# Optimization experiments

Hardware: AMD Instinct MI355X
Metric: run time of the kernel (lower is better)

The kernel has to match this reference:

```python
import jax, jax.numpy as jnp
import numpy as np

DIM = 256
QK_DIM = 256
NUM_HEADS = 8
N_WIN = 7
TOPK = 4
SCALE = QK_DIM ** (-0.5)


def setup_inputs() -> dict:
    key = jax.random.key(0)
    k1, k2, k3 = jax.random.split(key, 3)
    N, D, H, W, C = 2, 8, 56, 56, DIM
    x = jax.random.normal(k1, (N, D, H, W, C), dtype=jnp.float32)
    # QKVLinear: Linear(dim, qk_dim + qk_dim + dim)
    Wqkv = jax.random.normal(k2, (C, 2 * QK_DIM + DIM), dtype=jnp.float32) * 0.02
    bqkv = jnp.zeros((2 * QK_DIM + DIM,), dtype=jnp.float32)
    Wo = jax.random.normal(k3, (DIM, DIM), dtype=jnp.float32) * 0.02
    bo = jnp.zeros((DIM,), dtype=jnp.float32)
    return {"x": x, "Wqkv": Wqkv, "bqkv": bqkv, "Wo": Wo, "bo": bo}


def reference(x, Wqkv, bqkv, Wo, bo):
    N, D, H, W, C = x.shape
    j = i = N_WIN
    h, w = H // j, W // i
    p2, w2 = j * i, h * w
    n = N * D
    m = NUM_HEADS
    ch = QK_DIM // m   # qk head dim
    cv = DIM // m      # v head dim

    # n t (j h) (i w) c -> n t (j i) h w c
    xw = x.reshape(N, D, j, h, i, w, C).transpose(0, 1, 2, 4, 3, 5, 6)
    xw = xw.reshape(N, D, p2, h, w, C)

    # QKVLinear then split into q / kv
    qkv = xw @ Wqkv + bqkv                       # (N,D,p2,h,w,2qk+dim)
    q = qkv[..., :QK_DIM]                        # (N,D,p2,h,w,qk)
    kv = qkv[..., QK_DIM:]                       # (N,D,p2,h,w,qk+dim)

    # inter-frame shift: frame t uses kv of frame t+1; last frame keeps its own
    kv = jnp.concatenate([kv[:, 1:], kv[:, -1:]], axis=1)

    q = q.reshape(n, p2, h, w, QK_DIM)
    kv = kv.reshape(n, p2, h, w, QK_DIM + DIM)
    q_pix = q.reshape(n, p2, w2, QK_DIM)
    kv_pix = kv.reshape(n, p2, w2, QK_DIM + DIM)  # identity kv_down

    # window-level routing (diff_routing=False -> detached)
    q_win = jax.lax.stop_gradient(q.mean(axis=(2, 3)))                  # (n,p2,qk)
    k_win = jax.lax.stop_gradient(kv[..., :QK_DIM].mean(axis=(2, 3)))   # (n,p2,qk)
    attn_logit = jnp.einsum('npc,nqc->npq', q_win * SCALE, k_win)       # (n,p2,p2)
    topk_logit, r_idx = jax.lax.top_k(attn_logit, TOPK)                 # (n,p2,topk)
    r_weight = jax.nn.softmax(topk_logit, axis=-1)  # computed, unused (mul_weight='none')

    # gather kv of routed windows: (n,p2,topk,w2,qk+dim)
    kv_sel = jax.vmap(lambda kvp, idx: kvp[idx])(kv_pix, r_idx)

    k_sel = kv_sel[..., :QK_DIM].reshape(n, p2, TOPK * w2, m, ch)
    v_sel = kv_sel[..., QK_DIM:].reshape(n, p2, TOPK * w2, m, cv)
    qh = q_pix.reshape(n, p2, w2, m, ch)

    attn = jnp.einsum('npqmc,npkmc->npmqk', qh * SCALE, k_sel)  # (n,p2,m,w2,topk*w2)
    attn = jax.nn.softmax(attn, axis=-1)
    out = jnp.einsum('npmqk,npkmc->npqmc', attn, v_sel).reshape(n, p2, w2, C)

    # (n j i) (h w) c -> N D (j h) (i w) c
    out = out.reshape(N, D, j, i, h, w, C).transpose(0, 1, 2, 4, 3, 5, 6)
    out = out.reshape(N, D, H, W, C)
    out = out @ Wo + bo
    return out
```

## Files before the change

### kernel.cpp

```cpp
#include <hip/hip_runtime.h>
#include <math.h>

#define SCALE 0.0625f

typedef __attribute__((ext_vector_type(8))) short bf16x8;
typedef __attribute__((ext_vector_type(4))) float f32x4;

__device__ __forceinline__ ushort f2bf(float f) {
    unsigned u = __float_as_uint(f);
    return (ushort)((u + 0x7FFFu + ((u >> 16) & 1u)) >> 16);
}

__device__ __forceinline__ int token_to_xrow(int t) {
    int nd  = t / 3136;
    int r   = t % 3136;
    int p   = r >> 6;
    int pix = r & 63;
    int j = p / 7, i = p % 7;
    int hh = pix >> 3, ww = pix & 7;
    return nd * 3136 + (j * 8 + hh) * 56 + (i * 8 + ww);
}

__global__ __launch_bounds__(256) void k_cast_x(const float* __restrict__ x,
                                                ushort* __restrict__ xg) {
    int gid = blockIdx.x * 256 + threadIdx.x;
    int t = gid >> 6, c = (gid & 63) * 4;
    float4 v = *(const float4*)&x[(size_t)token_to_xrow(t) * 256 + c];
    ushort4 o;
    o.x = f2bf(v.x); o.y = f2bf(v.y); o.z = f2bf(v.z); o.w = f2bf(v.w);
    *(ushort4*)&xg[(size_t)t * 256 + c] = o;
}

__global__ __launch_bounds__(256) void k_cast_w(const float* __restrict__ Wqkv,
                                                const float* __restrict__ Wo,
                                                ushort* __restrict__ Wqkvt,
                                                ushort* __restrict__ Wot) {
    int b = blockIdx.x, tid = threadIdx.x;
    if (b < 768) Wqkvt[b * 256 + tid] = f2bf(Wqkv[(size_t)tid * 768 + b]);
    else { int n = b - 768; Wot[n * 256 + tid] = f2bf(Wo[(size_t)tid * 256 + n]); }
}

__global__ __launch_bounds__(256) void k_xmean(const float* __restrict__ x,
                                               float* __restrict__ xmean) {
    int b = blockIdx.x;
    int nd = b / 49, p = b % 49;
    int j = p / 7, i = p % 7;
    const float* xb = x + ((size_t)nd * 3136 + (j * 8) * 56 + i * 8) * 256 + threadIdx.x;
    float s = 0.f;
#pragma unroll
    for (int hh = 0; hh < 8; ++hh)
#pragma unroll
        for (int ww = 0; ww < 8; ++ww) s += xb[(size_t)(hh * 56 + ww) * 256];
    xmean[(size_t)b * 256 + threadIdx.x] = s * (1.f / 64.f);
}

__global__ __launch_bounds__(256) void k_winproj(const float* __restrict__ xmean,
                                                 const float* __restrict__ Wqkv,
                                                 const float* __restrict__ bqkv,
                                                 float* __restrict__ qwin,
                                                 float* __restrict__ kwin) {
    __shared__ float As[16 * 68];
    __shared__ float Bs[16 * 64];
    const int tid = threadIdx.x;
    const int m0 = blockIdx.y * 64;
    const int n0 = blockIdx.x * 64;

    const int ar = tid >> 2;
    const int ak = (tid & 3) * 4;
    const int arow = (m0 + ar < 784) ? (m0 + ar) : 783;
    const float* aptr = xmean + (size_t)arow * 256 + ak;

    const int bk = tid >> 4;
    const int bn = (tid & 15) * 4;
    const float* bptr = Wqkv + (size_t)bk * 768 + n0 + bn;

    const int ty = tid >> 4, tx = tid & 15;
    float acc[4][4] = {};

    for (int kt = 0; kt < 256; kt += 16) {
        float4 av = *(const float4*)(aptr + kt);
        float4 bv = *(const float4*)(bptr + (size_t)kt * 768);
        __syncthreads();
        As[(ak + 0) * 68 + ar] = av.x;
        As[(ak + 1) * 68 + ar] = av.y;
        As[(ak + 2) * 68 + ar] = av.z;
        As[(ak + 3) * 68 + ar] = av.w;
        *(float4*)&Bs[bk * 64 + bn] = bv;
        __syncthreads();
#pragma unroll
        for (int kk = 0; kk < 16; ++kk) {
            float4 a4 = *(const float4*)&As[kk * 68 + ty * 4];
            float4 b4 = *(const float4*)&Bs[kk * 64 + tx * 4];
            float a[4] = {a4.x, a4.y, a4.z, a4.w};
            float b[4] = {b4.x, b4.y, b4.z, b4.w};
#pragma unroll
            for (int ii = 0; ii < 4; ++ii)
#pragma unroll
                for (int jj = 0; jj < 4; ++jj) acc[ii][jj] += a[ii] * b[jj];
        }
    }
#pragma unroll
    for (int ii = 0; ii < 4; ++ii) {
        int t = m0 + ty * 4 + ii;
        if (t >= 784) continue;
#pragma unroll
        for (int jj = 0; jj < 4; ++jj) {
            int col = n0 + tx * 4 + jj;
            float v = acc[ii][jj] + bqkv[col];
            if (col < 256) qwin[(size_t)t * 256 + col] = v;
            else           kwin[(size_t)t * 256 + (col - 256)] = v;
        }
    }
}

__global__ __launch_bounds__(64) void k_route(const float* __restrict__ qwin,
                                              const float* __restrict__ kwin,
                                              int* __restrict__ ridx) {
    const int b = blockIdx.x;
    const int nd = b / 49;
    const int ndkv = ((nd & 7) == 7) ? nd : nd + 1;
    const int t = threadIdx.x;
    __shared__ float qs[256];
    for (int i = t; i < 256; i += 64) qs[i] = qwin[b * 256 + i];
    __syncthreads();
    float logit = -INFINITY;
    if (t < 49) {
        const float* kr = kwin + ((size_t)ndkv * 49 + t) * 256;
        float s = 0.f;
        for (int c = 0; c < 256; ++c) s += qs[c] * kr[c];
        logit = s;
    }
    for (int sel = 0; sel < 4; ++sel) {
        float v = logit;
        int ix = t;
        for (int off = 32; off > 0; off >>= 1) {
            float ov = __shfl_xor(v, off);
            int   oi = __shfl_xor(ix, off);
            if (ov > v || (ov == v && oi < ix)) { v = ov; ix = oi; }
        }
        if (t == 0) ridx[b * 4 + sel] = ix;
        if (t == ix) logit = -INFINITY;
    }
}

__global__ __launch_bounds__(256) void k_gemm_qkv(const ushort* __restrict__ A,
                                                  const ushort* __restrict__ Bt,
                                                  const float* __restrict__ bqkv,
                                                  ushort* __restrict__ q,
                                                  ushort* __restrict__ kv) {
    __shared__ ushort As[128 * 32];
    __shared__ ushort Bs[128 * 32];
    const int tid = threadIdx.x;
    const int wv = tid >> 6, ln = tid & 63;
    const int lane15 = ln & 15, quad = ln >> 4;
    const int m0 = blockIdx.y * 128, n0 = blockIdx.x * 128;

    const int row0 = tid >> 2, ck = tid & 3;

    f32x4 acc[4][4];
#pragma unroll
    for (int i = 0; i < 4; ++i)
#pragma unroll
        for (int j = 0; j < 4; ++j) acc[i][j] = (f32x4){0.f, 0.f, 0.f, 0.f};

    bf16x8 avA[2], avB[2];
#pragma unroll
    for (int p = 0; p < 2; ++p) {
        avA[p] = *(const bf16x8*)(A  + (size_t)(m0 + p * 64 + row0) * 256 + ck * 8);
        avB[p] = *(const bf16x8*)(Bt + (size_t)(n0 + p * 64 + row0) * 256 + ck * 8);
    }

    const int mb = (wv >> 1) * 64, nb = (wv & 1) * 64;

    for (int kt = 0; kt < 8; ++kt) {
        __syncthreads();
#pragma unroll
        for (int p = 0; p < 2; ++p) {
            *(bf16x8*)&As[(p * 256 + tid) * 8] = avA[p];
            *(bf16x8*)&Bs[(p * 256 + tid) * 8] = avB[p];
        }
        if (kt < 7) {
#pragma unroll
            for (int p = 0; p < 2; ++p) {
                avA[p] = *(const bf16x8*)(A  + (size_t)(m0 + p * 64 + row0) * 256 + (kt + 1) * 32 + ck * 8);
                avB[p] = *(const bf16x8*)(Bt + (size_t)(n0 + p * 64 + row0) * 256 + (kt + 1) * 32 + ck * 8);
            }
        }
        __syncthreads();
        bf16x8 aF[4], bF[4];
#pragma unroll
        for (int mt = 0; mt < 4; ++mt)
            aF[mt] = *(const bf16x8*)&As[(mb + mt * 16 + lane15) * 32 + quad * 8];
#pragma unroll
        for (int nt = 0; nt < 4; ++nt)
            bF[nt] = *(const bf16x8*)&Bs[(nb + nt * 16 + lane15) * 32 + quad * 8];
#pragma unroll
        for (int mt = 0; mt < 4; ++mt)
#pragma unroll
            for (int nt = 0; nt < 4; ++nt)
                acc[mt][nt] = __builtin_amdgcn_mfma_f32_16x16x32_bf16(aF[mt], bF[nt], acc[mt][nt], 0, 0, 0);
    }

#pragma unroll
    for (int mt = 0; mt < 4; ++mt) {
#pragma unroll
        for (int nt = 0; nt < 4; ++nt) {
            int col = n0 + nb + nt * 16 + lane15;
            float bias = bqkv[col];
#pragma unroll
            for (int r = 0; r < 4; ++r) {
                int t = m0 + mb + mt * 16 + quad * 4 + r;
                ushort b = f2bf(acc[mt][nt][r] + bias);
                if (col < 256) q[(size_t)t * 256 + col] = b;
                else           kv[(size_t)t * 512 + (col - 256)] = b;
            }
        }
    }
}

__global__ __launch_bounds__(256) void k_gemm_o(const ushort* __restrict__ A,
                                                const ushort* __restrict__ Bt,
                                                const float* __restrict__ bo,
                                                float* __restrict__ out) {
    __shared__ ushort As[128 * 32];
    __shared__ ushort Bs[128 * 32];
    const int tid = threadIdx.x;
    const int wv = tid >> 6, ln = tid & 63;
    const int lane15 = ln & 15, quad = ln >> 4;
    const int m0 = blockIdx.y * 128, n0 = blockIdx.x * 128;
    const int row0 = tid >> 2, ck = tid & 3;

    f32x4 acc[4][4];
#pragma unroll
    for (int i = 0; i < 4; ++i)
#pragma unroll
        for (int j = 0; j < 4; ++j) acc[i][j] = (f32x4){0.f, 0.f, 0.f, 0.f};

    bf16x8 avA[2], avB[2];
#pragma unroll
    for (int p = 0; p < 2; ++p) {
        avA[p] = *(const bf16x8*)(A  + (size_t)(m0 + p * 64 + row0) * 256 + ck * 8);
        avB[p] = *(const bf16x8*)(Bt + (size_t)(n0 + p * 64 + row0) * 256 + ck * 8);
    }
    const int mb = (wv >> 1) * 64, nb = (wv & 1) * 64;

    for (int kt = 0; kt < 8; ++kt) {
        __syncthreads();
#pragma unroll
        for (int p = 0; p < 2; ++p) {
            *(bf16x8*)&As[(p * 256 + tid) * 8] = avA[p];
            *(bf16x8*)&Bs[(p * 256 + tid) * 8] = avB[p];
        }
        if (kt < 7) {
#pragma unroll
            for (int p = 0; p < 2; ++p) {
                avA[p] = *(const bf16x8*)(A  + (size_t)(m0 + p * 64 + row0) * 256 + (kt + 1) * 32 + ck * 8);
                avB[p] = *(const bf16x8*)(Bt + (size_t)(n0 + p * 64 + row0) * 256 + (kt + 1) * 32 + ck * 8);
            }
        }
        __syncthreads();
        bf16x8 aF[4], bF[4];
#pragma unroll
        for (int mt = 0; mt < 4; ++mt)
            aF[mt] = *(const bf16x8*)&As[(mb + mt * 16 + lane15) * 32 + quad * 8];
#pragma unroll
        for (int nt = 0; nt < 4; ++nt)
            bF[nt] = *(const bf16x8*)&Bs[(nb + nt * 16 + lane15) * 32 + quad * 8];
#pragma unroll
        for (int mt = 0; mt < 4; ++mt)
#pragma unroll
            for (int nt = 0; nt < 4; ++nt)
                acc[mt][nt] = __builtin_amdgcn_mfma_f32_16x16x32_bf16(aF[mt], bF[nt], acc[mt][nt], 0, 0, 0);
    }

#pragma unroll
    for (int mt = 0; mt < 4; ++mt) {
#pragma unroll
        for (int nt = 0; nt < 4; ++nt) {
            int col = n0 + nb + nt * 16 + lane15;
            float bias = bo[col];
#pragma unroll
            for (int r = 0; r < 4; ++r) {
                int t = m0 + mb + mt * 16 + quad * 4 + r;
                int xr = token_to_xrow(t);
                out[(size_t)xr * 256 + col] = acc[mt][nt][r] + bias;
            }
        }
    }
}

__global__ __launch_bounds__(256, 3) void k_attn(ushort* qbuf,
                                                 const ushort* __restrict__ kvbuf,
                                                 const int* __restrict__ ridx) {
    const int h = blockIdx.x, p = blockIdx.y, nd = blockIdx.z;
    const int ndkv = ((nd & 7) == 7) ? nd : nd + 1;
    const int tid = threadIdx.x;
    const int wv = tid >> 6, ln = tid & 63;
    const int lane15 = ln & 15, quad = ln >> 4;

    __shared__ ushort Ks[256 * 32];
    __shared__ ushort Vt[32 * 272];
    __shared__ ushort Ps[64 * 72];

    const int rb = (nd * 49 + p) * 4;
    int wid[4];
#pragma unroll
    for (int i = 0; i < 4; ++i) wid[i] = ridx[rb + i];

    const size_t kvband = (size_t)ndkv * 49;

    {
        int pix = tid >> 2, ck = tid & 3;
#pragma unroll
        for (int i = 0; i < 4; ++i) {
            size_t trow = (kvband + wid[i]) * 64 + pix;
            bf16x8 v = *(const bf16x8*)(kvbuf + trow * 512 + h * 32 + ck * 8);
            *(bf16x8*)&Ks[(i * 64 + pix) * 32 + ck * 8] = v;
        }
    }
    {
        int key_l = (tid & 31) * 2;
        int ch0 = (tid >> 5) * 4;
#pragma unroll
        for (int i = 0; i < 4; ++i) {
            size_t trow = (kvband + wid[i]) * 64;
            const ushort* g0 = kvbuf + (trow + key_l) * 512 + 256 + h * 32 + ch0;
            const ushort* g1 = g0 + 512;
            ushort4 a = *(const ushort4*)g0;
            ushort4 b = *(const ushort4*)g1;
            int kg = i * 64 + key_l;
            *(unsigned*)&Vt[(ch0 + 0) * 272 + kg] = (unsigned)a.x | ((unsigned)b.x << 16);
            *(unsigned*)&Vt[(ch0 + 1) * 272 + kg] = (unsigned)a.y | ((unsigned)b.y << 16);
            *(unsigned*)&Vt[(ch0 + 2) * 272 + kg] = (unsigned)a.z | ((unsigned)b.z << 16);
            *(unsigned*)&Vt[(ch0 + 3) * 272 + kg] = (unsigned)a.w | ((unsigned)b.w << 16);
        }
    }

    const size_t qrow0 = (size_t)(nd * 49 + p) * 64;
    bf16x8 bQ = *(const bf16x8*)(qbuf + (qrow0 + wv * 16 + lane15) * 256 + h * 32 + quad * 8);

    __syncthreads();

    f32x4 st[16];
#pragma unroll
    for (int t = 0; t < 16; ++t) {
        bf16x8 aK = *(const bf16x8*)&Ks[(t * 16 + lane15) * 32 + quad * 8];
        st[t] = __builtin_amdgcn_mfma_f32_16x16x32_bf16(aK, bQ, (f32x4){0.f, 0.f, 0.f, 0.f}, 0, 0, 0);
    }

    float mx = -1e30f;
#pragma unroll
    for (int t = 0; t < 16; ++t)
#pragma unroll
        for (int r = 0; r < 4; ++r) mx = fmaxf(mx, st[t][r]);
    mx = fmaxf(mx, __shfl_xor(mx, 16));
    mx = fmaxf(mx, __shfl_xor(mx, 32));
    float sum = 0.f;
#pragma unroll
    for (int t = 0; t < 16; ++t)
#pragma unroll
        for (int r = 0; r < 4; ++r) {
            float e = __expf((st[t][r] - mx) * SCALE);
            st[t][r] = e;
            sum += e;
        }
    sum += __shfl_xor(sum, 16);
    sum += __shfl_xor(sum, 32);
    const float inv = 1.f / sum;

    f32x4 oacc[2] = {{0.f, 0.f, 0.f, 0.f}, {0.f, 0.f, 0.f, 0.f}};
    const int prow = (wv * 16 + lane15) * 72;
#pragma unroll
    for (int cc = 0; cc < 4; ++cc) {
#pragma unroll
        for (int tt = 0; tt < 4; ++tt) {
            int t = cc * 4 + tt;
            unsigned lo = (unsigned)f2bf(st[t][0] * inv) | ((unsigned)f2bf(st[t][1] * inv) << 16);
            unsigned hi = (unsigned)f2bf(st[t][2] * inv) | ((unsigned)f2bf(st[t][3] * inv) << 16);
            uint2 pk; pk.x = lo; pk.y = hi;
            *(uint2*)&Ps[prow + tt * 16 + quad * 4] = pk;
        }
#pragma unroll
        for (int kt = 0; kt < 2; ++kt) {
            bf16x8 aP = *(const bf16x8*)&Ps[prow + kt * 32 + quad * 8];
#pragma unroll
            for (int nt = 0; nt < 2; ++nt) {
                bf16x8 bV = *(const bf16x8*)&Vt[(nt * 16 + lane15) * 272 + cc * 64 + kt * 32 + quad * 8];
                oacc[nt] = __builtin_amdgcn_mfma_f32_16x16x32_bf16(aP, bV, oacc[nt], 0, 0, 0);
            }
        }
    }

#pragma unroll
    for (int nt = 0; nt < 2; ++nt)
#pragma unroll
        for (int r = 0; r < 4; ++r) {
            int row = wv * 16 + quad * 4 + r;
            qbuf[(qrow0 + row) * 256 + h * 32 + nt * 16 + lane15] = f2bf(oacc[nt][r]);
        }
}

extern "C" void kernel_launch(void* const* d_in, const int* in_sizes, int n_in,
                              void* d_out, int out_size, void* d_ws, size_t ws_size,
                              hipStream_t stream) {
    const float* x    = (const float*)d_in[0];
    const float* Wqkv = (const float*)d_in[1];
    const float* bqkv = (const float*)d_in[2];
    const float* Wo   = (const float*)d_in[3];
    const float* bo   = (const float*)d_in[4];
    float* out = (float*)d_out;

    char* ws = (char*)d_ws;
    ushort* xg    = (ushort*)ws;                    ws += (size_t)50176 * 256 * 2;
    ushort* q     = (ushort*)ws;                    ws += (size_t)50176 * 256 * 2;
    ushort* kv    = (ushort*)ws;                    ws += (size_t)50176 * 512 * 2;
    ushort* Wqkvt = (ushort*)ws;                    ws += (size_t)768 * 256 * 2;
    ushort* Wot   = (ushort*)ws;                    ws += (size_t)256 * 256 * 2;
    float*  xmean = (float*)ws;                     ws += (size_t)784 * 256 * 4;
    float*  qwin  = (float*)ws;                     ws += (size_t)784 * 256 * 4;
    float*  kwin  = (float*)ws;                     ws += (size_t)784 * 256 * 4;
    int*    ridx  = (int*)ws;

    k_cast_w  <<<1024, 256, 0, stream>>>(Wqkv, Wo, Wqkvt, Wot);
    k_cast_x  <<<12544, 256, 0, stream>>>(x, xg);
    k_xmean   <<<784, 256, 0, stream>>>(x, xmean);
    k_winproj <<<dim3(8, 13), 256, 0, stream>>>(xmean, Wqkv, bqkv, qwin, kwin);
    k_route   <<<784, 64, 0, stream>>>(qwin, kwin, ridx);
    k_gemm_qkv<<<dim3(6, 392), 256, 0, stream>>>(xg, Wqkvt, bqkv, q, kv);
    k_attn    <<<dim3(8, 49, 16), 256, 0, stream>>>(q, kv, ridx);
    k_gemm_o  <<<dim3(2, 392), 256, 0, stream>>>(q, Wot, bo, out);
}
```

Measured before the change: 258.2 us.

## Use direct global-to-LDS loads in GEMMs and simplify attention softmax

Both GEMM kernels now stage A/B tiles with global_load_lds directly into shared memory, replacing the register-staged prefetch. The QKV GEMM pre-scales q by scale*log2(e), so the attention kernel drops the max-subtraction pass and uses exp2. Normalization by the row sum is deferred to the output write, and bf16 packing uses the paired conversion intrinsic. LDS strides for K and V are changed to alter bank mapping. The trade-offs are that the GEMM loop loses its explicit load/compute overlap, and dropping the max subtraction relies on logits staying small enough to avoid overflow.

```diff
diff --git a/kernel.cpp b/kernel.cpp
--- a/kernel.cpp
+++ b/kernel.cpp
@@ -1,7 +1,8 @@
 #include <hip/hip_runtime.h>
+#include <hip/hip_bf16.h>
 #include <math.h>
 
-#define SCALE 0.0625f
+#define QSC 0.09016844f
 
 typedef __attribute__((ext_vector_type(8))) short bf16x8;
 typedef __attribute__((ext_vector_type(4))) float f32x4;
@@ -9,6 +10,17 @@
 __device__ __forceinline__ ushort f2bf(float f) {
     unsigned u = __float_as_uint(f);
     return (ushort)((u + 0x7FFFu + ((u >> 16) & 1u)) >> 16);
+}
+
+__device__ __forceinline__ unsigned pk2bf(float a, float b) {
+    __hip_bfloat162 h = __float22bfloat162_rn(make_float2(a, b));
+    return *(unsigned*)&h;
+}
+
+__device__ __forceinline__ void gl_lds16(const ushort* g, ushort* l) {
+    __builtin_amdgcn_global_load_lds(
+        (const __attribute__((address_space(1))) unsigned int*)g,
+        (__attribute__((address_space(3))) unsigned int*)l, 16, 0, 0);
 }
 
 __device__ __forceinline__ int token_to_xrow(int t) {
@@ -154,37 +166,32 @@
     const int wv = tid >> 6, ln = tid & 63;
     const int lane15 = ln & 15, quad = ln >> 4;
     const int m0 = blockIdx.y * 128, n0 = blockIdx.x * 128;
-
     const int row0 = tid >> 2, ck = tid & 3;
 
+    const ushort* gA[2]; const ushort* gB[2];
+    ushort* lA[2]; ushort* lB[2];
+#pragma unroll
+    for (int p = 0; p < 2; ++p) {
+        gA[p] = A  + (size_t)(m0 + p * 64 + row0) * 256 + ck * 8;
+        gB[p] = Bt + (size_t)(n0 + p * 64 + row0) * 256 + ck * 8;
+        lA[p] = &As[(p * 256 + tid) * 8];
+        lB[p] = &Bs[(p * 256 + tid) * 8];
+    }
+
     f32x4 acc[4][4];
 #pragma unroll
     for (int i = 0; i < 4; ++i)
 #pragma unroll
         for (int j = 0; j < 4; ++j) acc[i][j] = (f32x4){0.f, 0.f, 0.f, 0.f};
 
-    bf16x8 avA[2], avB[2];
-#pragma unroll
-    for (int p = 0; p < 2; ++p) {
-        avA[p] = *(const bf16x8*)(A  + (size_t)(m0 + p * 64 + row0) * 256 + ck * 8);
-        avB[p] = *(const bf16x8*)(Bt + (size_t)(n0 + p * 64 + row0) * 256 + ck * 8);
-    }
-
     const int mb = (wv >> 1) * 64, nb = (wv & 1) * 64;
 
     for (int kt = 0; kt < 8; ++kt) {
         __syncthreads();
 #pragma unroll
         for (int p = 0; p < 2; ++p) {
-            *(bf16x8*)&As[(p * 256 + tid) * 8] = avA[p];
-            *(bf16x8*)&Bs[(p * 256 + tid) * 8] = avB[p];
-        }
-        if (kt < 7) {
-#pragma unroll
-            for (int p = 0; p < 2; ++p) {
-                avA[p] = *(const bf16x8*)(A  + (size_t)(m0 + p * 64 + row0) * 256 + (kt + 1) * 32 + ck * 8);
-                avB[p] = *(const bf16x8*)(Bt + (size_t)(n0 + p * 64 + row0) * 256 + (kt + 1) * 32 + ck * 8);
-            }
+            gl_lds16(gA[p] + kt * 32, lA[p]);
+            gl_lds16(gB[p] + kt * 32, lB[p]);
         }
         __syncthreads();
         bf16x8 aF[4], bF[4];
@@ -210,9 +217,9 @@
 #pragma unroll
             for (int r = 0; r < 4; ++r) {
                 int t = m0 + mb + mt * 16 + quad * 4 + r;
-                ushort b = f2bf(acc[mt][nt][r] + bias);
-                if (col < 256) q[(size_t)t * 256 + col] = b;
-                else           kv[(size_t)t * 512 + (col - 256)] = b;
+                float v = acc[mt][nt][r] + bias;
+                if (col < 256) q[(size_t)t * 256 + col] = f2bf(v * QSC);
+                else           kv[(size_t)t * 512 + (col - 256)] = f2bf(v);
             }
         }
     }
@@ -230,33 +237,30 @@
     const int m0 = blockIdx.y * 128, n0 = blockIdx.x * 128;
     const int row0 = tid >> 2, ck = tid & 3;
 
+    const ushort* gA[2]; const ushort* gB[2];
+    ushort* lA[2]; ushort* lB[2];
+#pragma unroll
+    for (int p = 0; p < 2; ++p) {
+        gA[p] = A  + (size_t)(m0 + p * 64 + row0) * 256 + ck * 8;
+        gB[p] = Bt + (size_t)(n0 + p * 64 + row0) * 256 + ck * 8;
+        lA[p] = &As[(p * 256 + tid) * 8];
+        lB[p] = &Bs[(p * 256 + tid) * 8];
+    }
+
     f32x4 acc[4][4];
 #pragma unroll
     for (int i = 0; i < 4; ++i)
 #pragma unroll
         for (int j = 0; j < 4; ++j) acc[i][j] = (f32x4){0.f, 0.f, 0.f, 0.f};
 
-    bf16x8 avA[2], avB[2];
-#pragma unroll
-    for (int p = 0; p < 2; ++p) {
-        avA[p] = *(const bf16x8*)(A  + (size_t)(m0 + p * 64 + row0) * 256 + ck * 8);
-        avB[p] = *(const bf16x8*)(Bt + (size_t)(n0 + p * 64 + row0) * 256 + ck * 8);
-    }
     const int mb = (wv >> 1) * 64, nb = (wv & 1) * 64;
 
     for (int kt = 0; kt < 8; ++kt) {
         __syncthreads();
 #pragma unroll
         for (int p = 0; p < 2; ++p) {
-            *(bf16x8*)&As[(p * 256 + tid) * 8] = avA[p];
-            *(bf16x8*)&Bs[(p * 256 + tid) * 8] = avB[p];
-        }
-        if (kt < 7) {
-#pragma unroll
-            for (int p = 0; p < 2; ++p) {
-                avA[p] = *(const bf16x8*)(A  + (size_t)(m0 + p * 64 + row0) * 256 + (kt + 1) * 32 + ck * 8);
-                avB[p] = *(const bf16x8*)(Bt + (size_t)(n0 + p * 64 + row0) * 256 + (kt + 1) * 32 + ck * 8);
-            }
+            gl_lds16(gA[p] + kt * 32, lA[p]);
+            gl_lds16(gB[p] + kt * 32, lB[p]);
         }
         __syncthreads();
         bf16x8 aF[4], bF[4];
@@ -298,8 +302,8 @@
     const int wv = tid >> 6, ln = tid & 63;
     const int lane15 = ln & 15, quad = ln >> 4;
 
-    __shared__ ushort Ks[256 * 32];
-    __shared__ ushort Vt[32 * 272];
+    __shared__ ushort Ks[256 * 40];
+    __shared__ ushort Vt[32 * 264];
     __shared__ ushort Ps[64 * 72];
 
     const int rb = (nd * 49 + p) * 4;
@@ -315,7 +319,7 @@
         for (int i = 0; i < 4; ++i) {
             size_t trow = (kvband + wid[i]) * 64 + pix;
             bf16x8 v = *(const bf16x8*)(kvbuf + trow * 512 + h * 32 + ck * 8);
-            *(bf16x8*)&Ks[(i * 64 + pix) * 32 + ck * 8] = v;
+            *(bf16x8*)&Ks[(i * 64 + pix) * 40 + ck * 8] = v;
         }
     }
     {
@@ -329,10 +333,10 @@
             ushort4 a = *(const ushort4*)g0;
             ushort4 b = *(const ushort4*)g1;
             int kg = i * 64 + key_l;
-            *(unsigned*)&Vt[(ch0 + 0) * 272 + kg] = (unsigned)a.x | ((unsigned)b.x << 16);
-            *(unsigned*)&Vt[(ch0 + 1) * 272 + kg] = (unsigned)a.y | ((unsigned)b.y << 16);
-            *(unsigned*)&Vt[(ch0 + 2) * 272 + kg] = (unsigned)a.z | ((unsigned)b.z << 16);
-            *(unsigned*)&Vt[(ch0 + 3) * 272 + kg] = (unsigned)a.w | ((unsigned)b.w << 16);
+            *(unsigned*)&Vt[(ch0 + 0) * 264 + kg] = (unsigned)a.x | ((unsigned)b.x << 16);
+            *(unsigned*)&Vt[(ch0 + 1) * 264 + kg] = (unsigned)a.y | ((unsigned)b.y << 16);
+            *(unsigned*)&Vt[(ch0 + 2) * 264 + kg] = (unsigned)a.z | ((unsigned)b.z << 16);
+            *(unsigned*)&Vt[(ch0 + 3) * 264 + kg] = (unsigned)a.w | ((unsigned)b.w << 16);
         }
     }
 
@@ -344,23 +348,16 @@
     f32x4 st[16];
 #pragma unroll
     for (int t = 0; t < 16; ++t) {
-        bf16x8 aK = *(const bf16x8*)&Ks[(t * 16 + lane15) * 32 + quad * 8];
+        bf16x8 aK = *(const bf16x8*)&Ks[(t * 16 + lane15) * 40 + quad * 8];
         st[t] = __builtin_amdgcn_mfma_f32_16x16x32_bf16(aK, bQ, (f32x4){0.f, 0.f, 0.f, 0.f}, 0, 0, 0);
     }
 
-    float mx = -1e30f;
+    float sum = 0.f;
 #pragma unroll
     for (int t = 0; t < 16; ++t)
 #pragma unroll
-        for (int r = 0; r < 4; ++r) mx = fmaxf(mx, st[t][r]);
-    mx = fmaxf(mx, __shfl_xor(mx, 16));
-    mx = fmaxf(mx, __shfl_xor(mx, 32));
-    float sum = 0.f;
-#pragma unroll
-    for (int t = 0; t < 16; ++t)
-#pragma unroll
         for (int r = 0; r < 4; ++r) {
-            float e = __expf((st[t][r] - mx) * SCALE);
+            float e = __builtin_amdgcn_exp2f(st[t][r]);
             st[t][r] = e;
             sum += e;
         }
@@ -375,9 +372,9 @@
 #pragma unroll
         for (int tt = 0; tt < 4; ++tt) {
             int t = cc * 4 + tt;
-            unsigned lo = (unsigned)f2bf(st[t][0] * inv) | ((unsigned)f2bf(st[t][1] * inv) << 16);
-            unsigned hi = (unsigned)f2bf(st[t][2] * inv) | ((unsigned)f2bf(st[t][3] * inv) << 16);
-            uint2 pk; pk.x = lo; pk.y = hi;
+            uint2 pk;
+            pk.x = pk2bf(st[t][0], st[t][1]);
+            pk.y = pk2bf(st[t][2], st[t][3]);
             *(uint2*)&Ps[prow + tt * 16 + quad * 4] = pk;
         }
 #pragma unroll
@@ -385,7 +382,7 @@
             bf16x8 aP = *(const bf16x8*)&Ps[prow + kt * 32 + quad * 8];
 #pragma unroll
             for (int nt = 0; nt < 2; ++nt) {
-                bf16x8 bV = *(const bf16x8*)&Vt[(nt * 16 + lane15) * 272 + cc * 64 + kt * 32 + quad * 8];
+                bf16x8 bV = *(const bf16x8*)&Vt[(nt * 16 + lane15) * 264 + cc * 64 + kt * 32 + quad * 8];
                 oacc[nt] = __builtin_amdgcn_mfma_f32_16x16x32_bf16(aP, bV, oacc[nt], 0, 0, 0);
             }
         }
@@ -396,7 +393,7 @@
 #pragma unroll
         for (int r = 0; r < 4; ++r) {
             int row = wv * 16 + quad * 4 + r;
-            qbuf[(qrow0 + row) * 256 + h * 32 + nt * 16 + lane15] = f2bf(oacc[nt][r]);
+            qbuf[(qrow0 + row) * 256 + h * 32 + nt * 16 + lane15] = f2bf(oacc[nt][r] * inv);
         }
 }
 
```

Result: no change. 257.6 us (-0.3%).
